# Kernel optimization log

Hardware: AMD Instinct MI355X
Metric: run time of the kernel (lower is better)

Reference implementation:

```python
import jax, jax.numpy as jnp
import numpy as np

B, N, D, H = 2, 4096, 512, 8
HD = D // H

def setup_inputs() -> dict:
    key = jax.random.key(0)
    ks = jax.random.split(key, 5)
    s = 1.0 / np.sqrt(D)
    return {
        "x": jax.random.normal(ks[0], (B, N, D), dtype=jnp.float32),
        "W_qkv": jax.random.uniform(ks[1], (D, 3 * D), minval=-s, maxval=s, dtype=jnp.float32),
        "b_qkv": jax.random.uniform(ks[2], (3 * D,), minval=-s, maxval=s, dtype=jnp.float32),
        "W_out": jax.random.uniform(ks[3], (D, D), minval=-s, maxval=s, dtype=jnp.float32),
        "b_out": jax.random.uniform(ks[4], (D,), minval=-s, maxval=s, dtype=jnp.float32),
    }

def reference(x, W_qkv, b_qkv, W_out, b_out):
    Bq, Nq, Dq = x.shape
    scale = HD ** -0.5
    qkv = x @ W_qkv + b_qkv                      # [B,N,3D]
    qkv = qkv.reshape(Bq, Nq, 3, H, HD)
    q, k, v = (jnp.moveaxis(qkv[:, :, i], 2, 1) for i in range(3))  # [B,H,N,hd]
    attn = jnp.einsum('bhqd,bhkd->bhqk', q, k) * scale   # [B,H,N,N]
    causal = jnp.tril(jnp.ones((Nq, Nq), dtype=bool))
    attn = jnp.where(causal, attn, -jnp.inf)
    attn = jax.nn.softmax(attn, axis=-1)
    out = jnp.einsum('bhqk,bhkd->bhqd', attn, v)         # [B,H,N,hd]
    out = jnp.moveaxis(out, 1, 2).reshape(Bq, Nq, Dq)
    return out @ W_out + b_out
```

## Files before the change

kernel.cpp:

```cpp
#include <hip/hip_runtime.h>
#include <hip/hip_bf16.h>


typedef __bf16 bf16_t;
typedef __bf16 bf16x2 __attribute__((ext_vector_type(2)));
typedef __bf16 bf16x4 __attribute__((ext_vector_type(4)));
typedef __bf16 bf16x8 __attribute__((ext_vector_type(8)));
typedef float  f32x4  __attribute__((ext_vector_type(4)));
typedef unsigned int uint32x4 __attribute__((ext_vector_type(4)));

__device__ __forceinline__ void gload_lds16(const bf16_t* g, bf16_t* l) {
    __builtin_amdgcn_global_load_lds(
        (const __attribute__((address_space(1))) void*)g,
        (__attribute__((address_space(3))) void*)l, 16, 0, 0);
}


__device__ __forceinline__ void transpose_tile_body(
    const float* __restrict__ in, bf16_t* __restrict__ out, int N,
    int n0, int k0, int tid, bf16_t (*T)[72])
{
    #pragma unroll
    for (int pass = 0; pass < 4; ++pass) {
        int kk = pass * 16 + (tid >> 4), nn = (tid & 15) * 4;
        float4 v = *(const float4*)(in + (size_t)(k0 + kk) * N + n0 + nn);
        T[nn + 0][kk] = (bf16_t)v.x; T[nn + 1][kk] = (bf16_t)v.y;
        T[nn + 2][kk] = (bf16_t)v.z; T[nn + 3][kk] = (bf16_t)v.w;
    }
    __syncthreads();
    #pragma unroll
    for (int pass = 0; pass < 2; ++pass) {
        int n = pass * 32 + (tid >> 3), c8 = (tid & 7) * 8;
        *(bf16x8*)(out + (size_t)(n0 + n) * 512 + k0 + c8) = *(const bf16x8*)&T[n][c8];
    }
}

__global__ void prep_kernel(const float* __restrict__ x, bf16_t* __restrict__ xb,
                            const float* __restrict__ Wqkv, bf16_t* __restrict__ WqT,
                            const float* __restrict__ Wout, bf16_t* __restrict__ WoT)
{
    __shared__ bf16_t T[64][72];
    const int bid = blockIdx.x, tid = threadIdx.x;
    if (bid < 4096) {
        int i = bid * 256 + tid;
        float4 v = ((const float4*)x)[i];
        bf16x4 o;
        o[0] = (bf16_t)v.x; o[1] = (bf16_t)v.y; o[2] = (bf16_t)v.z; o[3] = (bf16_t)v.w;
        ((bf16x4*)xb)[i] = o;
    } else if (bid < 4288) {
        int idx = bid - 4096;
        transpose_tile_body(Wqkv, WqT, 1536, (idx % 24) * 64, (idx / 24) * 64, tid, T);
    } else {
        int idx = bid - 4288;
        transpose_tile_body(Wout, WoT, 512, (idx & 7) * 64, (idx >> 3) * 64, tid, T);
    }
}


template <int MODE, int TN>
__global__ __launch_bounds__(256) void gemm_bt(
    const bf16_t* __restrict__ A, const bf16_t* __restrict__ Bt,
    const float* __restrict__ bias,
    bf16_t* __restrict__ Qg, bf16_t* __restrict__ Kg, bf16_t* __restrict__ Vtp,
    float* __restrict__ Cout,
    const bf16_t* __restrict__ OP, const float* __restrict__ LP)
{
    constexpr int NI = (TN == 128) ? 4 : 2;
    constexpr int NS = 4;
    __shared__ bf16_t smem[128 * 64 + TN * 64];
    __shared__ float linv_s[(MODE == 1) ? 1024 : 1];
    bf16_t* As = smem;
    bf16_t* Bs = smem + 128 * 64;
    const int tid  = threadIdx.x;
    const int wid  = tid >> 6, lane = tid & 63, l16 = lane & 15, quad = lane >> 4;
    const int l8   = l16 & 7;
    const int wr   = (TN == 128) ? (wid >> 1) * 64 : wid * 32;
    const int wc   = (TN == 128) ? (wid & 1) * 64 : 0;

    int bx, by;
    {
        const int gx  = gridDim.x;
        const int nwg = gx * gridDim.y;
        const int lin = blockIdx.y * gx + blockIdx.x;
        const int cpx = nwg >> 3;
        const int nl  = (lin & 7) * cpx + (lin >> 3);
        bx = nl % gx; by = nl / gx;
    }
    const int m0   = by * 128, n0 = bx * TN;
    const int b8   = (m0 >> 12) * 8;
    const int nbase0 = m0 & 4095;

    if (MODE == 1) {
        #pragma unroll
        for (int q = 0; q < 4; ++q) {
            int idx = tid + q * 256;
            int hh = idx >> 7, row = idx & 127;
            const float* lp = LP + (size_t)(b8 + hh) * 4096 + nbase0 + row;
            float l = 0.f;
            #pragma unroll
            for (int sl = 0; sl < NS; ++sl) l += lp[(size_t)sl * 65536];
            linv_s[idx] = 1.0f / l;
        }
    }

    f32x4 acc[NI][4] = {};

    for (int kk = 0; kk < 512; kk += 64) {
        __syncthreads();
        if (MODE == 1) {
            const int hh = kk >> 6;
            const size_t obase = (size_t)(b8 + hh) * 262144;
            #pragma unroll
            for (int i = 0; i < 4; ++i) {
                int slot = tid + i * 256;
                int row = slot >> 3, cg = (slot & 7) ^ (row & 7);
                const bf16_t* op = OP + obase + (size_t)(nbase0 + row) * 64 + cg * 8;
                float s[8] = {};
                #pragma unroll
                for (int sl = 0; sl < NS; ++sl) {
                    bf16x8 v = *(const bf16x8*)(op + (size_t)sl * 4194304);
                    #pragma unroll
                    for (int j = 0; j < 8; ++j) s[j] += (float)v[j];
                }
                const float inv = linv_s[(hh << 7) + row];
                bf16x8 o8;
                #pragma unroll
                for (int j = 0; j < 8; ++j) o8[j] = (bf16_t)(s[j] * inv);
                *(bf16x8*)&As[slot * 8] = o8;
            }
        } else {
            #pragma unroll
            for (int i = 0; i < 4; ++i) {
                int slot = tid + i * 256;
                int row = slot >> 3, cg = (slot & 7) ^ (row & 7);
                gload_lds16(A + (size_t)(m0 + row) * 512 + kk + cg * 8,
                            (bf16_t*)((char*)As + ((i * 256 + (wid << 6)) << 4)));
            }
        }
        #pragma unroll
        for (int i = 0; i < TN / 32; ++i) {
            int slot = tid + i * 256;
            int row = slot >> 3, cg = (slot & 7) ^ (row & 7);
            gload_lds16(Bt + (size_t)(n0 + row) * 512 + kk + cg * 8,
                        (bf16_t*)((char*)Bs + ((i * 256 + (wid << 6)) << 4)));
        }
        __syncthreads();
        #pragma unroll
        for (int s = 0; s < 2; ++s) {
            const int sw = (s * 4 + quad);
            bf16x8 a[NI], b[4];
            #pragma unroll
            for (int i = 0; i < NI; ++i) {
                int row = wr + i * 16 + l16;
                a[i] = *(const bf16x8*)&As[(row * 8 + (sw ^ l8)) * 8];
            }
            #pragma unroll
            for (int j = 0; j < 4; ++j) {
                int row = wc + j * 16 + l16;
                b[j] = *(const bf16x8*)&Bs[(row * 8 + (sw ^ l8)) * 8];
            }
            #pragma unroll
            for (int i = 0; i < NI; ++i)
                #pragma unroll
                for (int j = 0; j < 4; ++j)
                    acc[i][j] = __builtin_amdgcn_mfma_f32_16x16x32_bf16(a[i], b[j], acc[i][j], 0, 0, 0);
        }
    }

    const float qscale = 0.18033688011112042f;

    if (MODE == 0) {
        __syncthreads();
        bf16_t* E = smem;
        const float qs = (n0 < 512) ? qscale : 1.0f;
        #pragma unroll
        for (int i = 0; i < NI; ++i) {
            #pragma unroll
            for (int j = 0; j < 4; ++j) {
                int col = wc + j * 16 + l16;
                float bv = bias[n0 + col];
                #pragma unroll
                for (int r = 0; r < 4; ++r) {
                    int row = wr + i * 16 + quad * 4 + r;
                    int sc = (((col >> 3) ^ (row & 15) ^ ((row >> 3) & 7)) << 3) + (col & 7);
                    E[row * 128 + sc] = (bf16_t)((acc[i][j][r] + bv) * qs);
                }
            }
        }
        __syncthreads();

        const int b_ = m0 >> 12;
        if (n0 < 1024) {
            bf16_t* dst = (n0 < 512) ? Qg : Kg;
            #pragma unroll
            for (int p = 0; p < 8; ++p) {
                int g = p * 256 + tid;
                int c = g & 7, drow = g >> 3;
                int hsel = drow >> 7, nl = drow & 127;
                int col0 = hsel * 64 + c * 8;
                int sc = (((col0 >> 3) ^ (nl & 15) ^ ((nl >> 3) & 7)) << 3);
                bf16x8 v = *(const bf16x8*)&E[nl * 128 + sc];
                int hh = ((n0 + hsel * 64) >> 6) & 7;
                int n = (m0 & 4095) + nl;
                size_t idx = (((size_t)(b_ * 8 + hh) * 4096) + n) * 64 + c * 8;
                *(bf16x8*)(dst + idx) = v;
            }
        } else {
            #pragma unroll
            for (int p = 0; p < 8; ++p) {
                int g = p * 256 + tid;
                int cn8 = g & 15, hdrow = g >> 4;
                int hsel = hdrow >> 6, hd = hdrow & 63;
                int col = hsel * 64 + hd;
                bf16x8 v;
                #pragma unroll
                for (int k = 0; k < 8; ++k) {
                    int row = cn8 * 8 + k;
                    int sc = (((col >> 3) ^ (row & 15) ^ ((row >> 3) & 7)) << 3) + (col & 7);
                    v[k] = E[row * 128 + sc];
                }
                int hh = ((n0 + hsel * 64) >> 6) & 7;
                int nbase = (m0 & 4095) + cn8 * 8;
                size_t idx = ((size_t)(b_ * 8 + hh) * 64 + hd) * 4096 + nbase;
                *(bf16x8*)(Vtp + idx) = v;
            }
        }
    } else {
        #pragma unroll
        for (int i = 0; i < NI; ++i) {
            int mrow = m0 + wr + i * 16 + quad * 4;
            #pragma unroll
            for (int j = 0; j < 4; ++j) {
                int cgl = n0 + wc + j * 16 + l16;
                float bv = bias[cgl];
                #pragma unroll
                for (int r = 0; r < 4; ++r) {
                    int m = mrow + r;
                    Cout[(size_t)m * 512 + cgl] = acc[i][j][r] + bv;
                }
            }
        }
    }
}


__global__ __launch_bounds__(256, 2) void attn_ns2(
    const bf16_t* __restrict__ Qg, const bf16_t* __restrict__ Kg,
    const bf16_t* __restrict__ Vt,
    bf16_t* __restrict__ o_part, float* __restrict__ l_part, int nsplit)
{
    __shared__ bf16_t Ks[2][64][72];
    __shared__ bf16_t Vs[2][64][72];

    const int tid  = threadIdx.x;
    const int w    = tid >> 6, lane = tid & 63, l16 = lane & 15, quad = lane >> 4;
    const int bh   = blockIdx.x & 15, pr = (blockIdx.x >> 4) & 7, h = blockIdx.x >> 7;

    bf16_t* ob = o_part + (size_t)(h * 16 + bh) * 4096 * 64;
    float*  lb = l_part + (size_t)(h * 16 + bh) * 4096;

    const int srow = tid >> 3, scol = (tid & 7) * 8;
    const int srow1 = srow + 32;
    const float MSHIFT = 12.0f;

    bf16x8 ones;
    #pragma unroll
    for (int j = 0; j < 8; ++j) ones[j] = (bf16_t)1.0f;

    uint4 kr0, kr1, vr0, vr1;

#define TILE_PROLOGUE()                                                        \
    const int cur = kt & 1;                                                    \
    *(uint4*)&Ks[cur][srow][scol]  = kr0;                                      \
    *(uint4*)&Ks[cur][srow1][scol] = kr1;                                      \
    *(uint4*)&Vs[cur][srow][scol]  = vr0;                                      \
    *(uint4*)&Vs[cur][srow1][scol] = vr1;                                      \
    __syncthreads();                                                           \
    if (kt + 1 < b1) {                                                         \
        const size_t kb = ((size_t)bh * 4096 + (kt + 1) * 64) * 64;            \
        const size_t vb = (size_t)bh * 64 * 4096 + (kt + 1) * 64;              \
        kr0 = *(const uint4*)(Kg + kb + (size_t)srow * 64 + scol);             \
        kr1 = *(const uint4*)(Kg + kb + (size_t)srow1 * 64 + scol);            \
        vr0 = *(const uint4*)(Vt + vb + (size_t)srow * 4096 + scol);           \
        vr1 = *(const uint4*)(Vt + vb + (size_t)srow1 * 4096 + scol);          \
    }                                                                          \
    bf16x8 kf[4][2], vf[4][2];                                                 \
    _Pragma("unroll")                                                          \
    for (int cb = 0; cb < 4; ++cb) {                                           \
        kf[cb][0] = *(const bf16x8*)&Ks[cur][cb * 16 + l16][quad * 8];         \
        kf[cb][1] = *(const bf16x8*)&Ks[cur][cb * 16 + l16][32 + quad * 8];    \
    }                                                                          \
    _Pragma("unroll")                                                          \
    for (int j = 0; j < 4; ++j) {                                              \
        vf[j][0] = *(const bf16x8*)&Vs[cur][j * 16 + l16][quad * 8];           \
        vf[j][1] = *(const bf16x8*)&Vs[cur][j * 16 + l16][32 + quad * 8];      \
    }

#define SOFTMAX_PERMLANE(sv, pa0, pa1)                                         \
    unsigned int c_[4][2];                                                     \
    _Pragma("unroll")                                                          \
    for (int cb = 0; cb < 4; ++cb) {                                           \
        _Pragma("unroll")                                                      \
        for (int t = 0; t < 2; ++t) {                                          \
            bf16x2 pk2;                                                        \
            pk2[0] = (bf16_t)__builtin_amdgcn_exp2f(sv[cb][2 * t]     - MSHIFT); \
            pk2[1] = (bf16_t)__builtin_amdgcn_exp2f(sv[cb][2 * t + 1] - MSHIFT); \
            c_[cb][t] = __builtin_bit_cast(unsigned int, pk2);                 \
        }                                                                      \
    }                                                                          \
    unsigned int pw0[4], pw1[4];                                               \
    _Pragma("unroll")                                                          \
    for (int t = 0; t < 2; ++t) {                                              \
        auto u  = __builtin_amdgcn_permlane32_swap(c_[0][t], c_[1][t], false, false); \
        auto z  = __builtin_amdgcn_permlane16_swap(u[0], u[1], false, false);  \
        pw0[t] = z[0]; pw0[t + 2] = z[1];                                      \
        auto u2 = __builtin_amdgcn_permlane32_swap(c_[2][t], c_[3][t], false, false); \
        auto z2 = __builtin_amdgcn_permlane16_swap(u2[0], u2[1], false, false); \
        pw1[t] = z2[0]; pw1[t + 2] = z2[1];                                    \
    }                                                                          \
    uint32x4 w0v = {pw0[0], pw0[1], pw0[2], pw0[3]};                           \
    uint32x4 w1v = {pw1[0], pw1[1], pw1[2], pw1[3]};                           \
    bf16x8 pa0 = __builtin_bit_cast(bf16x8, w0v);                              \
    bf16x8 pa1 = __builtin_bit_cast(bf16x8, w1v);

    for (int ph = 0; ph < 2; ++ph) {
        const int st = ph ? (15 - pr) : pr;
        const int T  = 4 * st + 4;
        const int b0 = (h * T) / nsplit, b1 = ((h + 1) * T) / nsplit;
        const int st4 = 4 * st;
        const int fastEnd = (st4 < b1) ? st4 : b1;

        int qrow[4];
        bf16x8 qf[4][2];
        #pragma unroll
        for (int s = 0; s < 4; ++s) {
            qrow[s] = st * 256 + s * 64 + w * 16 + l16;
            const bf16_t* qp = Qg + ((size_t)bh * 4096 + qrow[s]) * 64;
            qf[s][0] = *(const bf16x8*)(qp + quad * 8);
            qf[s][1] = *(const bf16x8*)(qp + 32 + quad * 8);
        }

        f32x4 o[4][4] = {};
        f32x4 lacc[4] = {};

        {
            const size_t kb = ((size_t)bh * 4096 + b0 * 64) * 64;
            const size_t vb = (size_t)bh * 64 * 4096 + b0 * 64;
            kr0 = *(const uint4*)(Kg + kb + (size_t)srow * 64 + scol);
            kr1 = *(const uint4*)(Kg + kb + (size_t)srow1 * 64 + scol);
            vr0 = *(const uint4*)(Vt + vb + (size_t)srow * 4096 + scol);
            vr1 = *(const uint4*)(Vt + vb + (size_t)srow1 * 4096 + scol);
        }
        __syncthreads();

        int kt = b0;

        for (; kt < fastEnd; ++kt) {
            TILE_PROLOGUE();
            #pragma unroll
            for (int s = 0; s < 4; ++s) {
                f32x4 sv[4] = {};
                __builtin_amdgcn_s_setprio(1);
                #pragma unroll
                for (int cb = 0; cb < 4; ++cb) {
                    sv[cb] = __builtin_amdgcn_mfma_f32_16x16x32_bf16(kf[cb][0], qf[s][0], sv[cb], 0, 0, 0);
                    sv[cb] = __builtin_amdgcn_mfma_f32_16x16x32_bf16(kf[cb][1], qf[s][1], sv[cb], 0, 0, 0);
                }
                __builtin_amdgcn_s_setprio(0);
                SOFTMAX_PERMLANE(sv, pa0, pa1);
                __builtin_amdgcn_s_setprio(1);
                #pragma unroll
                for (int j = 0; j < 4; ++j) {
                    o[s][j] = __builtin_amdgcn_mfma_f32_16x16x32_bf16(pa0, vf[j][0], o[s][j], 0, 0, 0);
                    o[s][j] = __builtin_amdgcn_mfma_f32_16x16x32_bf16(pa1, vf[j][1], o[s][j], 0, 0, 0);
                }
                lacc[s] = __builtin_amdgcn_mfma_f32_16x16x32_bf16(pa0, ones, lacc[s], 0, 0, 0);
                lacc[s] = __builtin_amdgcn_mfma_f32_16x16x32_bf16(pa1, ones, lacc[s], 0, 0, 0);
                __builtin_amdgcn_s_setprio(0);
            }
        }

        for (; kt < b1; ++kt) {
            TILE_PROLOGUE();
            #pragma unroll
            for (int s = 0; s < 4; ++s) {
                const int diag = st4 + s;
                if (kt > diag) continue;

                f32x4 sv[4] = {};
                #pragma unroll
                for (int cb = 0; cb < 4; ++cb) {
                    sv[cb] = __builtin_amdgcn_mfma_f32_16x16x32_bf16(kf[cb][0], qf[s][0], sv[cb], 0, 0, 0);
                    sv[cb] = __builtin_amdgcn_mfma_f32_16x16x32_bf16(kf[cb][1], qf[s][1], sv[cb], 0, 0, 0);
                }

                if (kt == diag) {
                    #pragma unroll
                    for (int cb = 0; cb < 4; ++cb) {
                        const int keyg = kt * 64 + cb * 16 + quad * 4;
                        #pragma unroll
                        for (int r = 0; r < 4; ++r)
                            if (keyg + r > qrow[s]) sv[cb][r] = -1e30f;
                    }
                }

                SOFTMAX_PERMLANE(sv, pa0, pa1);
                #pragma unroll
                for (int j = 0; j < 4; ++j) {
                    o[s][j] = __builtin_amdgcn_mfma_f32_16x16x32_bf16(pa0, vf[j][0], o[s][j], 0, 0, 0);
                    o[s][j] = __builtin_amdgcn_mfma_f32_16x16x32_bf16(pa1, vf[j][1], o[s][j], 0, 0, 0);
                }
                lacc[s] = __builtin_amdgcn_mfma_f32_16x16x32_bf16(pa0, ones, lacc[s], 0, 0, 0);
                lacc[s] = __builtin_amdgcn_mfma_f32_16x16x32_bf16(pa1, ones, lacc[s], 0, 0, 0);
            }
        }

        #pragma unroll
        for (int s = 0; s < 4; ++s)
            #pragma unroll
            for (int r = 0; r < 4; ++r) {
                int n = st * 256 + s * 64 + w * 16 + quad * 4 + r;
                #pragma unroll
                for (int j = 0; j < 4; ++j)
                    ob[(size_t)n * 64 + j * 16 + l16] = (bf16_t)o[s][j][r];
                if (l16 == 0) lb[n] = lacc[s][r];
            }
    }
#undef TILE_PROLOGUE
#undef SOFTMAX_PERMLANE
}


extern "C" void kernel_launch(void* const* d_in, const int* in_sizes, int n_in,
                              void* d_out, int out_size, void* d_ws, size_t ws_size,
                              hipStream_t stream) {
    const float* x    = (const float*)d_in[0];
    const float* Wqkv = (const float*)d_in[1];
    const float* bqkv = (const float*)d_in[2];
    const float* Wout = (const float*)d_in[3];
    const float* bout = (const float*)d_in[4];
    float* out = (float*)d_out;

    char* ws = (char*)d_ws;
    bf16_t* xb  = (bf16_t*)(ws);
    bf16_t* WqT = (bf16_t*)(ws + 8388608);
    bf16_t* WoT = (bf16_t*)(ws + 9961472);
    bf16_t* Qg  = (bf16_t*)(ws + 10485760);
    bf16_t* Kg  = (bf16_t*)(ws + 18874368);
    bf16_t* Vt  = (bf16_t*)(ws + 27262976);

    const int nsplit = 4;
    bf16_t* o_part = (bf16_t*)(ws + 35651584);
    float*  l_part = (float*)(ws + 35651584 + (size_t)nsplit * 8388608);

    prep_kernel<<<4352, 256, 0, stream>>>(x, xb, Wqkv, WqT, Wout, WoT);

    gemm_bt<0, 128><<<dim3(12, 64), 256, 0, stream>>>(
        xb, WqT, bqkv, Qg, Kg, Vt, nullptr, nullptr, nullptr);

    attn_ns2<<<128 * nsplit, 256, 0, stream>>>(Qg, Kg, Vt, o_part, l_part, nsplit);

    gemm_bt<1, 128><<<dim3(4, 64), 256, 0, stream>>>(
        nullptr, WoT, bout, nullptr, nullptr, nullptr, out, o_part, l_part);
}
```

Measured before the change: 173.3 us.

## Prefetch split partials into registers, fold softmax shift into MFMA init, retile output GEMM

The output-projection GEMM now loads the next head's split-K attention partials into registers while the current tile is computed, so the global-load latency overlaps with MFMA work instead of sitting on the critical path. In the attention kernel, the constant max shift is folded into the score accumulator's initial value, which removes a subtraction per element before exp2. The s_setprio priority toggles are dropped. The output GEMM also moves from 128-wide to 64-wide N tiles with twice as many blocks, which raises parallelism but makes each block re-read and re-reduce the partials, and the prefetch increases register pressure.

```diff
diff --git a/kernel.cpp b/kernel.cpp
--- a/kernel.cpp
+++ b/kernel.cpp
@@ -90,6 +90,8 @@
     const int b8   = (m0 >> 12) * 8;
     const int nbase0 = m0 & 4095;
 
+    bf16x8 aw[4][NS];
+
     if (MODE == 1) {
         #pragma unroll
         for (int q = 0; q < 4; ++q) {
@@ -101,6 +103,16 @@
             for (int sl = 0; sl < NS; ++sl) l += lp[(size_t)sl * 65536];
             linv_s[idx] = 1.0f / l;
         }
+        const size_t obase = (size_t)b8 * 262144;
+        #pragma unroll
+        for (int i = 0; i < 4; ++i) {
+            int slot = tid + i * 256;
+            int row = slot >> 3, cg = (slot & 7) ^ (row & 7);
+            const bf16_t* op = OP + obase + (size_t)(nbase0 + row) * 64 + cg * 8;
+            #pragma unroll
+            for (int sl = 0; sl < NS; ++sl)
+                aw[i][sl] = *(const bf16x8*)(op + (size_t)sl * 4194304);
+        }
     }
 
     f32x4 acc[NI][4] = {};
@@ -108,24 +120,27 @@
     for (int kk = 0; kk < 512; kk += 64) {
         __syncthreads();
         if (MODE == 1) {
+            #pragma unroll
+            for (int i = 0; i < TN / 32; ++i) {
+                int slot = tid + i * 256;
+                int row = slot >> 3, cg = (slot & 7) ^ (row & 7);
+                gload_lds16(Bt + (size_t)(n0 + row) * 512 + kk + cg * 8,
+                            (bf16_t*)((char*)Bs + ((i * 256 + (wid << 6)) << 4)));
+            }
             const int hh = kk >> 6;
-            const size_t obase = (size_t)(b8 + hh) * 262144;
             #pragma unroll
             for (int i = 0; i < 4; ++i) {
                 int slot = tid + i * 256;
-                int row = slot >> 3, cg = (slot & 7) ^ (row & 7);
-                const bf16_t* op = OP + obase + (size_t)(nbase0 + row) * 64 + cg * 8;
-                float s[8] = {};
-                #pragma unroll
-                for (int sl = 0; sl < NS; ++sl) {
-                    bf16x8 v = *(const bf16x8*)(op + (size_t)sl * 4194304);
+                int row = slot >> 3;
+                float s8[8] = {};
+                #pragma unroll
+                for (int sl = 0; sl < NS; ++sl)
                     #pragma unroll
-                    for (int j = 0; j < 8; ++j) s[j] += (float)v[j];
-                }
+                    for (int j = 0; j < 8; ++j) s8[j] += (float)aw[i][sl][j];
                 const float inv = linv_s[(hh << 7) + row];
                 bf16x8 o8;
                 #pragma unroll
-                for (int j = 0; j < 8; ++j) o8[j] = (bf16_t)(s[j] * inv);
+                for (int j = 0; j < 8; ++j) o8[j] = (bf16_t)(s8[j] * inv);
                 *(bf16x8*)&As[slot * 8] = o8;
             }
         } else {
@@ -136,15 +151,30 @@
                 gload_lds16(A + (size_t)(m0 + row) * 512 + kk + cg * 8,
                             (bf16_t*)((char*)As + ((i * 256 + (wid << 6)) << 4)));
             }
-        }
-        #pragma unroll
-        for (int i = 0; i < TN / 32; ++i) {
-            int slot = tid + i * 256;
-            int row = slot >> 3, cg = (slot & 7) ^ (row & 7);
-            gload_lds16(Bt + (size_t)(n0 + row) * 512 + kk + cg * 8,
-                        (bf16_t*)((char*)Bs + ((i * 256 + (wid << 6)) << 4)));
+            #pragma unroll
+            for (int i = 0; i < TN / 32; ++i) {
+                int slot = tid + i * 256;
+                int row = slot >> 3, cg = (slot & 7) ^ (row & 7);
+                gload_lds16(Bt + (size_t)(n0 + row) * 512 + kk + cg * 8,
+                            (bf16_t*)((char*)Bs + ((i * 256 + (wid << 6)) << 4)));
+            }
         }
         __syncthreads();
+
+        if (MODE == 1 && kk + 64 < 512) {
+            const int hh2 = (kk >> 6) + 1;
+            const size_t obase = (size_t)(b8 + hh2) * 262144;
+            #pragma unroll
+            for (int i = 0; i < 4; ++i) {
+                int slot = tid + i * 256;
+                int row = slot >> 3, cg = (slot & 7) ^ (row & 7);
+                const bf16_t* op = OP + obase + (size_t)(nbase0 + row) * 64 + cg * 8;
+                #pragma unroll
+                for (int sl = 0; sl < NS; ++sl)
+                    aw[i][sl] = *(const bf16x8*)(op + (size_t)sl * 4194304);
+            }
+        }
+
         #pragma unroll
         for (int s = 0; s < 2; ++s) {
             const int sw = (s * 4 + quad);
@@ -303,8 +333,8 @@
         _Pragma("unroll")                                                      \
         for (int t = 0; t < 2; ++t) {                                          \
             bf16x2 pk2;                                                        \
-            pk2[0] = (bf16_t)__builtin_amdgcn_exp2f(sv[cb][2 * t]     - MSHIFT); \
-            pk2[1] = (bf16_t)__builtin_amdgcn_exp2f(sv[cb][2 * t + 1] - MSHIFT); \
+            pk2[0] = (bf16_t)__builtin_amdgcn_exp2f(sv[cb][2 * t]);            \
+            pk2[1] = (bf16_t)__builtin_amdgcn_exp2f(sv[cb][2 * t + 1]);        \
             c_[cb][t] = __builtin_bit_cast(unsigned int, pk2);                 \
         }                                                                      \
     }                                                                          \
@@ -359,16 +389,16 @@
             TILE_PROLOGUE();
             #pragma unroll
             for (int s = 0; s < 4; ++s) {
-                f32x4 sv[4] = {};
-                __builtin_amdgcn_s_setprio(1);
+                f32x4 sv[4];
+                #pragma unroll
+                for (int cb = 0; cb < 4; ++cb)
+                    sv[cb] = f32x4{-MSHIFT, -MSHIFT, -MSHIFT, -MSHIFT};
                 #pragma unroll
                 for (int cb = 0; cb < 4; ++cb) {
                     sv[cb] = __builtin_amdgcn_mfma_f32_16x16x32_bf16(kf[cb][0], qf[s][0], sv[cb], 0, 0, 0);
                     sv[cb] = __builtin_amdgcn_mfma_f32_16x16x32_bf16(kf[cb][1], qf[s][1], sv[cb], 0, 0, 0);
                 }
-                __builtin_amdgcn_s_setprio(0);
                 SOFTMAX_PERMLANE(sv, pa0, pa1);
-                __builtin_amdgcn_s_setprio(1);
                 #pragma unroll
                 for (int j = 0; j < 4; ++j) {
                     o[s][j] = __builtin_amdgcn_mfma_f32_16x16x32_bf16(pa0, vf[j][0], o[s][j], 0, 0, 0);
@@ -376,7 +406,6 @@
                 }
                 lacc[s] = __builtin_amdgcn_mfma_f32_16x16x32_bf16(pa0, ones, lacc[s], 0, 0, 0);
                 lacc[s] = __builtin_amdgcn_mfma_f32_16x16x32_bf16(pa1, ones, lacc[s], 0, 0, 0);
-                __builtin_amdgcn_s_setprio(0);
             }
         }
 
@@ -387,7 +416,10 @@
                 const int diag = st4 + s;
                 if (kt > diag) continue;
 
-                f32x4 sv[4] = {};
+                f32x4 sv[4];
+                #pragma unroll
+                for (int cb = 0; cb < 4; ++cb)
+                    sv[cb] = f32x4{-MSHIFT, -MSHIFT, -MSHIFT, -MSHIFT};
                 #pragma unroll
                 for (int cb = 0; cb < 4; ++cb) {
                     sv[cb] = __builtin_amdgcn_mfma_f32_16x16x32_bf16(kf[cb][0], qf[s][0], sv[cb], 0, 0, 0);
@@ -460,6 +492,6 @@
 
     attn_ns2<<<128 * nsplit, 256, 0, stream>>>(Qg, Kg, Vt, o_part, l_part, nsplit);
 
-    gemm_bt<1, 128><<<dim3(4, 64), 256, 0, stream>>>(
+    gemm_bt<1, 64><<<dim3(8, 64), 256, 0, stream>>>(
         nullptr, WoT, bout, nullptr, nullptr, nullptr, out, o_part, l_part);
 }
```

Result: faster. 162.5 us (-6.3%).
